# Optimization experiments

Measured on AMD Instinct MI355X. Metric: run time of the kernel, lower is better.

## Reference

```python
import jax, jax.numpy as jnp
import numpy as np
import math

D = 768
SCALE = math.sqrt(D)


def setup_inputs() -> dict:
    key = jax.random.key(0)
    k1, k2, k3, k4 = jax.random.split(key, 4)
    lhs = jax.random.normal(k1, (8, 1024, D), dtype=jnp.float32)
    rhs = jax.random.normal(k2, (8, 1024, D), dtype=jnp.float32)
    # xavier_normal_ std = sqrt(2/(fan_in+fan_out))
    std = math.sqrt(2.0 / (D + D))
    W_lhs = jax.random.normal(k3, (D, D), dtype=jnp.float32) * std
    W_rhs = jax.random.normal(k4, (D, D), dtype=jnp.float32) * std
    return {"lhs": lhs, "rhs": rhs, "W_lhs": W_lhs, "W_rhs": W_rhs}


def reference(lhs, rhs, W_lhs, W_rhs):
    # Linear (no bias): x @ W.T, then tanh
    l = jnp.tanh(jnp.einsum('nld,ed->nle', lhs, W_lhs))  # (N, L, D)
    r = jnp.tanh(jnp.einsum('nrd,ed->nre', rhs, W_rhs))  # (N, R, D)
    scores = jnp.einsum('nld,nrd->nlr', l, r)            # (N, L, R)
    attn_lhs = jax.nn.softmax(scores, axis=2)            # unscaled, row softmax
    attn_rhs = jax.nn.softmax(scores / SCALE, axis=1)    # scaled, column softmax
    out_lhs = jnp.einsum('nlr,nrd->nld', attn_lhs, rhs)
    out_rhs = jnp.einsum('nlr,nld->nrd', attn_rhs, lhs)
    return (jnp.concatenate([lhs, out_lhs], axis=2),
            jnp.concatenate([rhs, out_rhs], axis=2))
```

## Files before the change

kernel.cpp:

```cpp
#include <hip/hip_runtime.h>

typedef _Float16 f16_t;
typedef _Float16 f16x4 __attribute__((ext_vector_type(4)));
typedef _Float16 f16x8 __attribute__((ext_vector_type(8)));
typedef short s16x8 __attribute__((ext_vector_type(8)));
typedef unsigned short u16x4 __attribute__((ext_vector_type(4)));
typedef float floatx4 __attribute__((ext_vector_type(4)));

#define NB 8
#define SEQ 1024
#define DIM 768
#define INV_SCALE 0.03608439182435161f
#define ROW_SHIFT 40.0f

__device__ inline unsigned short f2bf(float f) {
  unsigned u = __builtin_bit_cast(unsigned, f);
  u += 0x7fffu + ((u >> 16) & 1u);
  return (unsigned short)(u >> 16);
}

__device__ inline void async_load16(const void* g, void* l) {
  __builtin_amdgcn_global_load_lds((__attribute__((address_space(1))) void*)g,
                                   (__attribute__((address_space(3))) void*)l,
                                   16, 0, 0);
}


__global__ __launch_bounds__(256) void prep(
    const float* __restrict__ lhs, const float* __restrict__ rhs,
    const float* __restrict__ Wl, const float* __restrict__ Wr,
    f16_t* __restrict__ lf, f16_t* __restrict__ rf, f16_t* __restrict__ lhsT,
    unsigned short* __restrict__ rhsT, f16_t* __restrict__ Wlh,
    f16_t* __restrict__ Wrh, float* __restrict__ o0, float* __restrict__ o1) {
  const int z = blockIdx.z;
  const int tid = threadIdx.x;
  const int x4 = (tid & 15) * 4, ty = tid >> 4;
  const int c0 = blockIdx.x * 64, r0 = blockIdx.y * 64;
  if (z >= 16) {
    if (blockIdx.y >= 12) return;
    const float* in = (z == 17 ? Wr : Wl);
    f16_t* out = (z == 17 ? Wrh : Wlh);
    #pragma unroll
    for (int it = 0; it < 4; ++it) {
      const int row = r0 + ty + it * 16;
      const float4 v = *(const float4*)&in[(size_t)row * DIM + c0 + x4];
      f16x4 h = {(f16_t)v.x, (f16_t)v.y, (f16_t)v.z, (f16_t)v.w};
      *(f16x4*)&out[(size_t)row * DIM + c0 + x4] = h;
    }
    return;
  }
  __shared__ float tile[64][65];
  const int n = z & 7;
  const float* in = (z < 8 ? lhs : rhs) + (size_t)n * SEQ * DIM;
  f16_t* fout = (z < 8 ? lf : rf) + (size_t)n * SEQ * DIM;
  float* oh = (z < 8 ? o0 : o1) + (size_t)n * SEQ * 2 * DIM;
  #pragma unroll
  for (int it = 0; it < 4; ++it) {
    const int row = ty + it * 16;
    const float4 v = *(const float4*)&in[(size_t)(r0 + row) * DIM + c0 + x4];
    f16x4 h = {(f16_t)v.x, (f16_t)v.y, (f16_t)v.z, (f16_t)v.w};
    *(f16x4*)&fout[(size_t)(r0 + row) * DIM + c0 + x4] = h;
    *(float4*)&oh[(size_t)(r0 + row) * 2 * DIM + c0 + x4] = v;
    tile[row][x4 + 0] = v.x;
    tile[row][x4 + 1] = v.y;
    tile[row][x4 + 2] = v.z;
    tile[row][x4 + 3] = v.w;
  }
  __syncthreads();
  if (z < 8) {
    f16_t* T = lhsT + (size_t)n * SEQ * DIM;
    #pragma unroll
    for (int it = 0; it < 4; ++it) {
      const int cr = ty + it * 16;
      f16x4 o = {(f16_t)tile[x4 + 0][cr], (f16_t)tile[x4 + 1][cr],
                 (f16_t)tile[x4 + 2][cr], (f16_t)tile[x4 + 3][cr]};
      *(f16x4*)&T[(size_t)(c0 + cr) * SEQ + r0 + x4] = o;
    }
  } else {
    unsigned short* T = rhsT + (size_t)n * SEQ * DIM;
    #pragma unroll
    for (int it = 0; it < 4; ++it) {
      const int cr = ty + it * 16;
      u16x4 o = {f2bf(tile[x4 + 0][cr]), f2bf(tile[x4 + 1][cr]),
                 f2bf(tile[x4 + 2][cr]), f2bf(tile[x4 + 3][cr])};
      *(u16x4*)&T[(size_t)(c0 + cr) * SEQ + r0 + x4] = o;
    }
  }
}

__global__ __launch_bounds__(256, 3) void gemm_proj(
    const f16_t* __restrict__ A0, const f16_t* __restrict__ W0,
    const f16_t* __restrict__ A1, const f16_t* __restrict__ W1,
    f16_t* __restrict__ C0, f16_t* __restrict__ C1) {
  __shared__ __align__(16) f16_t sA[128 * 64];
  __shared__ __align__(16) f16_t sB[128 * 64];
  const int b = blockIdx.x;
  const int n = b & 7;
  const int s = b >> 3;
  const int side = s / 48;
  const int t = s - side * 48;
  const int j = t >> 3, myb = t & 7;
  const int my = n * 8 + myb;
  const f16_t* Ab = (side ? A1 : A0) + (size_t)my * 128 * DIM;
  const f16_t* Bb = (side ? W1 : W0) + (size_t)j * 128 * DIM;
  f16_t* C = side ? C1 : C0;
  const int tid = threadIdx.x;
  const int lane = tid & 63;
  const int wave = tid >> 6;
  const int wr = wave >> 1, wc = wave & 1;
  const int fr = lane & 15;
  const int fq = lane >> 4;
  const int swz = ((lane & 7) ^ (lane >> 3)) << 3;
  const int x7 = (fr & 7) << 3;

  floatx4 acc[4][4] = {};

  for (int kt = 0; kt < DIM; kt += 64) {
    #pragma unroll
    for (int i = 0; i < 4; ++i) {
      const int ch = i * 4 + wave;
      const int row = ch * 8 + (lane >> 3);
      const size_t g = (size_t)row * DIM + kt + swz;
      async_load16(Ab + g, (char*)sA + ch * 1024);
      async_load16(Bb + g, (char*)sB + ch * 1024);
    }
    __syncthreads();
    #pragma unroll
    for (int ks = 0; ks < 64; ks += 32) {
      f16x8 af[4], bf[4];
      #pragma unroll
      for (int t2 = 0; t2 < 4; ++t2) {
        const int cs = (ks + fq * 8) ^ x7;
        af[t2] = *(const f16x8*)&sA[(wr * 64 + t2 * 16 + fr) * 64 + cs];
        bf[t2] = *(const f16x8*)&sB[(wc * 64 + t2 * 16 + fr) * 64 + cs];
      }
      #pragma unroll
      for (int ti = 0; ti < 4; ++ti)
        #pragma unroll
        for (int tj = 0; tj < 4; ++tj)
          acc[ti][tj] = __builtin_amdgcn_mfma_f32_16x16x32_f16(
              af[ti], bf[tj], acc[ti][tj], 0, 0, 0);
    }
    __syncthreads();
  }

  const size_t m0 = (size_t)my * 128, n0 = (size_t)j * 128;
  #pragma unroll
  for (int ti = 0; ti < 4; ++ti)
    #pragma unroll
    for (int tj = 0; tj < 4; ++tj) {
      const size_t gm = m0 + wr * 64 + ti * 16 + fq * 4;
      const size_t gn = n0 + wc * 64 + tj * 16 + fr;
      #pragma unroll
      for (int i = 0; i < 4; ++i) {
        const float e = __expf(2.f * acc[ti][tj][i]);
        C[(gm + i) * DIM + gn] =
            (f16_t)(1.f - 2.f * __builtin_amdgcn_rcpf(e + 1.f));
      }
    }
}

__global__ __launch_bounds__(256, 3) void gemm_scores(
    const f16_t* __restrict__ A, const f16_t* __restrict__ B,
    unsigned short* __restrict__ e_l, f16_t* __restrict__ e_rT,
    float* __restrict__ rowpart, float* __restrict__ colpart) {
  __shared__ __align__(16) char smem[32768];
  const int b = blockIdx.x;
  const int tid = threadIdx.x;
  f16_t* sA = (f16_t*)smem;
  f16_t* sB = sA + 8192;
  const int z = b & 7;
  const int s = b >> 3;
  const int my = s >> 3, j = s & 7;
  const f16_t* Ab = A + (size_t)z * SEQ * DIM + (size_t)my * 128 * DIM;
  const f16_t* Bb = B + (size_t)z * SEQ * DIM + (size_t)j * 128 * DIM;
  const int lane = tid & 63;
  const int wave = tid >> 6;
  const int wr = wave >> 1, wc = wave & 1;
  const int fr = lane & 15;
  const int fq = lane >> 4;
  const int swz = ((lane & 7) ^ (lane >> 3)) << 3;
  const int x7 = (fr & 7) << 3;

  floatx4 acc[4][4] = {};

  for (int kt = 0; kt < DIM; kt += 64) {
    #pragma unroll
    for (int i = 0; i < 4; ++i) {
      const int ch = i * 4 + wave;
      const int row = ch * 8 + (lane >> 3);
      const size_t g = (size_t)row * DIM + kt + swz;
      async_load16(Ab + g, (char*)sA + ch * 1024);
      async_load16(Bb + g, (char*)sB + ch * 1024);
    }
    __syncthreads();
    #pragma unroll
    for (int ks = 0; ks < 64; ks += 32) {
      f16x8 af[4], bf[4];
      #pragma unroll
      for (int t2 = 0; t2 < 4; ++t2) {
        const int cs = (ks + fq * 8) ^ x7;
        af[t2] = *(const f16x8*)&sA[(wr * 64 + t2 * 16 + fr) * 64 + cs];
        bf[t2] = *(const f16x8*)&sB[(wc * 64 + t2 * 16 + fr) * 64 + cs];
      }
      #pragma unroll
      for (int ti = 0; ti < 4; ++ti)
        #pragma unroll
        for (int tj = 0; tj < 4; ++tj)
          acc[ti][tj] = __builtin_amdgcn_mfma_f32_16x16x32_f16(
              af[ti], bf[tj], acc[ti][tj], 0, 0, 0);
    }
    __syncthreads();
  }

  const size_t m0 = (size_t)my * 128, n0 = (size_t)j * 128;
  unsigned short* eL = e_l + (size_t)z * SEQ * SEQ;
  f16_t* eT = e_rT + (size_t)z * SEQ * SEQ;

  #pragma unroll
  for (int ti = 0; ti < 4; ++ti) {
    #pragma unroll
    for (int i = 0; i < 4; ++i) {
      const int rloc = wr * 64 + ti * 16 + fq * 4 + i;
      float sum = 0.f;
      #pragma unroll
      for (int tj = 0; tj < 4; ++tj) {
        const float e = __expf(acc[ti][tj][i] - ROW_SHIFT);
        sum += e;
        eL[(m0 + rloc) * SEQ + n0 + wc * 64 + tj * 16 + fr] = f2bf(e);
      }
      sum += __shfl_xor(sum, 1, 64);
      sum += __shfl_xor(sum, 2, 64);
      sum += __shfl_xor(sum, 4, 64);
      sum += __shfl_xor(sum, 8, 64);
      if (fr == 0)
        rowpart[((size_t)(z * 16 + j * 2 + wc)) * SEQ + m0 + rloc] = sum;
    }
  }
  #pragma unroll
  for (int tj = 0; tj < 4; ++tj) {
    const int rp = wc * 64 + tj * 16 + fr;
    float sum = 0.f;
    #pragma unroll
    for (int ti = 0; ti < 4; ++ti) {
      #pragma unroll
      for (int i = 0; i < 4; ++i) {
        const float e = __expf(acc[ti][tj][i] * INV_SCALE);
        sum += e;
        const int cp = wr * 64 + ti * 16 + fq * 4 + i;
        *(f16_t*)(smem + rp * 256 + ((cp * 2) ^ ((rp & 7) << 4))) = (f16_t)e;
      }
    }
    sum += __shfl_xor(sum, 16, 64);
    sum += __shfl_xor(sum, 32, 64);
    if (fq == 0)
      colpart[((size_t)(z * 16 + my * 2 + wr)) * SEQ + n0 + rp] = sum;
  }
  __syncthreads();
  #pragma unroll
  for (int it = 0; it < 8; ++it) {
    const int r = it * 16 + (tid >> 4), chunk = tid & 15;
    const f16x8 v =
        *(const f16x8*)(smem + r * 256 + ((chunk * 16) ^ ((r & 7) << 4)));
    *(f16x8*)&eT[(n0 + r) * SEQ + m0 + chunk * 8] = v;
  }
}

template <bool BF>
__device__ __forceinline__ void apply_body(
    const f16_t* __restrict__ Ab, const f16_t* __restrict__ Bb,
    float* __restrict__ C, const float* __restrict__ pp, f16_t* sA, f16_t* sB,
    float* sinv) {
  const int tid = threadIdx.x;
  const int lane = tid & 63;
  const int wave = tid >> 6;
  const int wr = wave >> 1, wc = wave & 1;
  const int fr = lane & 15;
  const int fq = lane >> 4;
  const int swz = ((lane & 7) ^ (lane >> 3)) << 3;
  const int x7 = (fr & 7) << 3;

  if (tid < 128) {
    float s = 0.f;
    #pragma unroll
    for (int k = 0; k < 16; ++k) s += pp[k * SEQ + tid];
    sinv[tid] = 1.f / s;
  }

  floatx4 acc[4][4] = {};

  for (int kt = 0; kt < SEQ; kt += 64) {
    #pragma unroll
    for (int i = 0; i < 4; ++i) {
      const int ch = i * 4 + wave;
      const int row = ch * 8 + (lane >> 3);
      const size_t g = (size_t)row * SEQ + kt + swz;
      async_load16(Ab + g, (char*)sA + ch * 1024);
      async_load16(Bb + g, (char*)sB + ch * 1024);
    }
    __syncthreads();
    #pragma unroll
    for (int ks = 0; ks < 64; ks += 32) {
      const int cs = (ks + fq * 8) ^ x7;
      #pragma unroll
      for (int ti = 0; ti < 4; ++ti) {
        const f16_t* pa = &sA[(wr * 64 + ti * 16 + fr) * 64 + cs];
        #pragma unroll
        for (int tj = 0; tj < 4; ++tj) {
          const f16_t* pb = &sB[(wc * 64 + tj * 16 + fr) * 64 + cs];
          if constexpr (BF)
            acc[ti][tj] = __builtin_amdgcn_mfma_f32_16x16x32_bf16(
                *(const s16x8*)pa, *(const s16x8*)pb, acc[ti][tj], 0, 0, 0);
          else
            acc[ti][tj] = __builtin_amdgcn_mfma_f32_16x16x32_f16(
                *(const f16x8*)pa, *(const f16x8*)pb, acc[ti][tj], 0, 0, 0);
        }
      }
    }
    __syncthreads();
  }

  #pragma unroll
  for (int ti = 0; ti < 4; ++ti) {
    const int gm = wr * 64 + ti * 16 + fq * 4;
    const floatx4 iv = *(const floatx4*)&sinv[gm];
    #pragma unroll
    for (int tj = 0; tj < 4; ++tj) {
      const int gn = wc * 64 + tj * 16 + fr;
      #pragma unroll
      for (int i = 0; i < 4; ++i)
        C[(size_t)(gm + i) * (2 * DIM) + gn] = acc[ti][tj][i] * iv[i];
    }
  }
}

__global__ __launch_bounds__(256, 3) void gemm_apply(
    const f16_t* __restrict__ e_l, const f16_t* __restrict__ e_rT,
    const f16_t* __restrict__ rhsT, const f16_t* __restrict__ lhsT,
    const float* __restrict__ rowpart, const float* __restrict__ colpart,
    float* __restrict__ out0, float* __restrict__ out1) {
  __shared__ __align__(16) f16_t sA[128 * 64];
  __shared__ __align__(16) f16_t sB[128 * 64];
  __shared__ __align__(16) float sinv[128];
  const int b = blockIdx.x;
  const int n = b & 7;
  const int s = b >> 3;
  const int side = s / 48;
  const int t = s - side * 48;
  const int j = t >> 3, my = t & 7;
  const size_t m0 = (size_t)my * 128, n0 = (size_t)j * 128;
  if (side == 0) {
    apply_body<true>(e_l + (size_t)n * SEQ * SEQ + m0 * SEQ,
                     rhsT + (size_t)n * SEQ * DIM + n0 * SEQ,
                     out0 + (size_t)n * SEQ * 2 * DIM + DIM + m0 * 2 * DIM + n0,
                     rowpart + (size_t)n * 16 * SEQ + m0, sA, sB, sinv);
  } else {
    apply_body<false>(
        e_rT + (size_t)n * SEQ * SEQ + m0 * SEQ,
        lhsT + (size_t)n * SEQ * DIM + n0 * SEQ,
        out1 + (size_t)n * SEQ * 2 * DIM + DIM + m0 * 2 * DIM + n0,
        colpart + (size_t)n * 16 * SEQ + m0, sA, sB, sinv);
  }
}

extern "C" void kernel_launch(void* const* d_in, const int* in_sizes, int n_in,
                              void* d_out, int out_size, void* d_ws,
                              size_t ws_size, hipStream_t stream) {
  const float* lhs = (const float*)d_in[0];
  const float* rhs = (const float*)d_in[1];
  const float* Wl = (const float*)d_in[2];
  const float* Wr = (const float*)d_in[3];
  float* out0 = (float*)d_out;
  float* out1 = out0 + (size_t)NB * SEQ * (2 * DIM);

  char* ws = (char*)d_ws;
  f16_t* lhsT = (f16_t*)(ws + 0);
  unsigned short* rhsT = (unsigned short*)(ws + 12582912);
  f16_t* l_f = (f16_t*)(ws + 25165824);
  f16_t* r_f = (f16_t*)(ws + 37748736);
  f16_t* lhs_f = (f16_t*)(ws + 50331648);
  f16_t* rhs_f = (f16_t*)(ws + 62914560);
  f16_t* Wl_h = (f16_t*)(ws + 75497472);
  f16_t* Wr_h = (f16_t*)(ws + 76677120);
  unsigned short* e_l = (unsigned short*)(ws + 50331648);
  f16_t* e_rT = (f16_t*)(ws + 67108864);
  float* rowpart = (float*)(ws + 83886080);
  float* colpart = (float*)(ws + 84410368);

  prep<<<dim3(12, 16, 18), 256, 0, stream>>>(lhs, rhs, Wl, Wr, lhs_f, rhs_f,
                                             lhsT, rhsT, Wl_h, Wr_h, out0,
                                             out1);
  gemm_proj<<<768, 256, 0, stream>>>(lhs_f, Wl_h, rhs_f, Wr_h, l_f, r_f);
  gemm_scores<<<512, 256, 0, stream>>>(l_f, r_f, e_l, e_rT, rowpart, colpart);
  gemm_apply<<<768, 256, 0, stream>>>((const f16_t*)e_l, e_rT,
                                      (const f16_t*)rhsT, lhsT, rowpart,
                                      colpart, out0, out1);
}
```

Before: 233.9 us.

## Fuse four kernels into one persistent megakernel with grid barriers

Result: slower. 515.5 us (+120.4%).

```diff
diff --git a/kernel.cpp b/kernel.cpp
--- a/kernel.cpp
+++ b/kernel.cpp
@@ -10,6 +10,7 @@
 #define NB 8
 #define SEQ 1024
 #define DIM 768
+#define NBLK 768
 #define INV_SCALE 0.03608439182435161f
 #define ROW_SHIFT 40.0f
 
@@ -25,85 +26,35 @@
                                    16, 0, 0);
 }
 
-
-__global__ __launch_bounds__(256) void prep(
+__device__ inline void grid_barrier(unsigned* sync, int phase) {
+  __syncthreads();
+  if (threadIdx.x == 0) {
+    __threadfence();
+    const unsigned arrived = atomicAdd(&sync[phase * 2], 1u);
+    if (arrived == NBLK - 1) {
+      atomicExch(&sync[phase * 2 + 1], 1u);
+    } else {
+      while (atomicOr(&sync[phase * 2 + 1], 0u) == 0u)
+        __builtin_amdgcn_s_sleep(8);
+    }
+    __threadfence();
+  }
+  __syncthreads();
+}
+
+__global__ __launch_bounds__(256, 3) void mega(
     const float* __restrict__ lhs, const float* __restrict__ rhs,
     const float* __restrict__ Wl, const float* __restrict__ Wr,
-    f16_t* __restrict__ lf, f16_t* __restrict__ rf, f16_t* __restrict__ lhsT,
-    unsigned short* __restrict__ rhsT, f16_t* __restrict__ Wlh,
-    f16_t* __restrict__ Wrh, float* __restrict__ o0, float* __restrict__ o1) {
-  const int z = blockIdx.z;
-  const int tid = threadIdx.x;
-  const int x4 = (tid & 15) * 4, ty = tid >> 4;
-  const int c0 = blockIdx.x * 64, r0 = blockIdx.y * 64;
-  if (z >= 16) {
-    if (blockIdx.y >= 12) return;
-    const float* in = (z == 17 ? Wr : Wl);
-    f16_t* out = (z == 17 ? Wrh : Wlh);
-    #pragma unroll
-    for (int it = 0; it < 4; ++it) {
-      const int row = r0 + ty + it * 16;
-      const float4 v = *(const float4*)&in[(size_t)row * DIM + c0 + x4];
-      f16x4 h = {(f16_t)v.x, (f16_t)v.y, (f16_t)v.z, (f16_t)v.w};
-      *(f16x4*)&out[(size_t)row * DIM + c0 + x4] = h;
-    }
-    return;
-  }
-  __shared__ float tile[64][65];
-  const int n = z & 7;
-  const float* in = (z < 8 ? lhs : rhs) + (size_t)n * SEQ * DIM;
-  f16_t* fout = (z < 8 ? lf : rf) + (size_t)n * SEQ * DIM;
-  float* oh = (z < 8 ? o0 : o1) + (size_t)n * SEQ * 2 * DIM;
-  #pragma unroll
-  for (int it = 0; it < 4; ++it) {
-    const int row = ty + it * 16;
-    const float4 v = *(const float4*)&in[(size_t)(r0 + row) * DIM + c0 + x4];
-    f16x4 h = {(f16_t)v.x, (f16_t)v.y, (f16_t)v.z, (f16_t)v.w};
-    *(f16x4*)&fout[(size_t)(r0 + row) * DIM + c0 + x4] = h;
-    *(float4*)&oh[(size_t)(r0 + row) * 2 * DIM + c0 + x4] = v;
-    tile[row][x4 + 0] = v.x;
-    tile[row][x4 + 1] = v.y;
-    tile[row][x4 + 2] = v.z;
-    tile[row][x4 + 3] = v.w;
-  }
-  __syncthreads();
-  if (z < 8) {
-    f16_t* T = lhsT + (size_t)n * SEQ * DIM;
-    #pragma unroll
-    for (int it = 0; it < 4; ++it) {
-      const int cr = ty + it * 16;
-      f16x4 o = {(f16_t)tile[x4 + 0][cr], (f16_t)tile[x4 + 1][cr],
-                 (f16_t)tile[x4 + 2][cr], (f16_t)tile[x4 + 3][cr]};
-      *(f16x4*)&T[(size_t)(c0 + cr) * SEQ + r0 + x4] = o;
-    }
-  } else {
-    unsigned short* T = rhsT + (size_t)n * SEQ * DIM;
-    #pragma unroll
-    for (int it = 0; it < 4; ++it) {
-      const int cr = ty + it * 16;
-      u16x4 o = {f2bf(tile[x4 + 0][cr]), f2bf(tile[x4 + 1][cr]),
-                 f2bf(tile[x4 + 2][cr]), f2bf(tile[x4 + 3][cr])};
-      *(u16x4*)&T[(size_t)(c0 + cr) * SEQ + r0 + x4] = o;
-    }
-  }
-}
-
-__global__ __launch_bounds__(256, 3) void gemm_proj(
-    const f16_t* __restrict__ A0, const f16_t* __restrict__ W0,
-    const f16_t* __restrict__ A1, const f16_t* __restrict__ W1,
-    f16_t* __restrict__ C0, f16_t* __restrict__ C1) {
-  __shared__ __align__(16) f16_t sA[128 * 64];
-  __shared__ __align__(16) f16_t sB[128 * 64];
-  const int b = blockIdx.x;
-  const int n = b & 7;
-  const int s = b >> 3;
-  const int side = s / 48;
-  const int t = s - side * 48;
-  const int j = t >> 3, myb = t & 7;
-  const int my = n * 8 + myb;
-  const f16_t* Ab = (side ? A1 : A0) + (size_t)my * 128 * DIM;
-  const f16_t* Bb = (side ? W1 : W0) + (size_t)j * 128 * DIM;
-  f16_t* C = side ? C1 : C0;
+    f16_t* __restrict__ lhs_f, f16_t* __restrict__ rhs_f,
+    f16_t* __restrict__ Wl_h, f16_t* __restrict__ Wr_h,
+    f16_t* __restrict__ lhsT, unsigned short* __restrict__ rhsT,
+    f16_t* __restrict__ l_f, f16_t* __restrict__ r_f,
+    unsigned short* __restrict__ e_l, f16_t* __restrict__ e_rT,
+    float* __restrict__ rowpart, float* __restrict__ colpart,
+    float* __restrict__ out0, float* __restrict__ out1, unsigned* sync) {
+  __shared__ __align__(16) char smem[32768];
+  __shared__ __align__(16) float sinv[128];
+  const int bid = blockIdx.x;
   const int tid = threadIdx.x;
   const int lane = tid & 63;
   const int wave = tid >> 6;
@@ -113,253 +64,290 @@
   const int swz = ((lane & 7) ^ (lane >> 3)) << 3;
   const int x7 = (fr & 7) << 3;
 
-  floatx4 acc[4][4] = {};
-
-  for (int kt = 0; kt < DIM; kt += 64) {
-    #pragma unroll
-    for (int i = 0; i < 4; ++i) {
-      const int ch = i * 4 + wave;
-      const int row = ch * 8 + (lane >> 3);
-      const size_t g = (size_t)row * DIM + kt + swz;
-      async_load16(Ab + g, (char*)sA + ch * 1024);
-      async_load16(Bb + g, (char*)sB + ch * 1024);
+  {
+    const int x4 = (tid & 15) * 4, ty = tid >> 4;
+    float(*tile)[65] = (float(*)[65])smem;
+    for (int v = bid; v < 3456; v += NBLK) {
+      const int z = v / 192;
+      const int rem = v - z * 192;
+      const int by = rem / 12, bx = rem - by * 12;
+      const int c0 = bx * 64, r0 = by * 64;
+      if (z >= 16) {
+        if (by < 12) {
+          const float* in = (z == 17 ? Wr : Wl);
+          f16_t* outp = (z == 17 ? Wr_h : Wl_h);
+          #pragma unroll
+          for (int it = 0; it < 4; ++it) {
+            const int row = r0 + ty + it * 16;
+            const float4 v4 = *(const float4*)&in[(size_t)row * DIM + c0 + x4];
+            *(f16x4*)&outp[(size_t)row * DIM + c0 + x4] =
+                f16x4{(f16_t)v4.x, (f16_t)v4.y, (f16_t)v4.z, (f16_t)v4.w};
+          }
+        }
+      } else {
+        const int n = z & 7;
+        const float* in = (z < 8 ? lhs : rhs) + (size_t)n * SEQ * DIM;
+        f16_t* fout = (z < 8 ? lhs_f : rhs_f) + (size_t)n * SEQ * DIM;
+        float* oh = (z < 8 ? out0 : out1) + (size_t)n * SEQ * 2 * DIM;
+        #pragma unroll
+        for (int it = 0; it < 4; ++it) {
+          const int row = ty + it * 16;
+          const float4 v4 =
+              *(const float4*)&in[(size_t)(r0 + row) * DIM + c0 + x4];
+          *(f16x4*)&fout[(size_t)(r0 + row) * DIM + c0 + x4] =
+              f16x4{(f16_t)v4.x, (f16_t)v4.y, (f16_t)v4.z, (f16_t)v4.w};
+          *(float4*)&oh[(size_t)(r0 + row) * 2 * DIM + c0 + x4] = v4;
+          tile[row][x4 + 0] = v4.x;
+          tile[row][x4 + 1] = v4.y;
+          tile[row][x4 + 2] = v4.z;
+          tile[row][x4 + 3] = v4.w;
+        }
+        __syncthreads();
+        if (z < 8) {
+          f16_t* T = lhsT + (size_t)n * SEQ * DIM;
+          #pragma unroll
+          for (int it = 0; it < 4; ++it) {
+            const int cr = ty + it * 16;
+            f16x4 o = {(f16_t)tile[x4 + 0][cr], (f16_t)tile[x4 + 1][cr],
+                       (f16_t)tile[x4 + 2][cr], (f16_t)tile[x4 + 3][cr]};
+            *(f16x4*)&T[(size_t)(c0 + cr) * SEQ + r0 + x4] = o;
+          }
+        } else {
+          unsigned short* T = rhsT + (size_t)n * SEQ * DIM;
+          #pragma unroll
+          for (int it = 0; it < 4; ++it) {
+            const int cr = ty + it * 16;
+            u16x4 o = {f2bf(tile[x4 + 0][cr]), f2bf(tile[x4 + 1][cr]),
+                       f2bf(tile[x4 + 2][cr]), f2bf(tile[x4 + 3][cr])};
+            *(u16x4*)&T[(size_t)(c0 + cr) * SEQ + r0 + x4] = o;
+          }
+        }
+      }
+      __syncthreads();
+    }
+  }
+  grid_barrier(sync, 0);
+
+  {
+    f16_t* sA = (f16_t*)smem;
+    f16_t* sB = sA + 8192;
+    const int n = bid & 7;
+    const int s = bid >> 3;
+    const int side = s / 48;
+    const int t = s - side * 48;
+    const int j = t >> 3, myb = t & 7;
+    const int my = n * 8 + myb;
+    const f16_t* Ab = (side ? rhs_f : lhs_f) + (size_t)my * 128 * DIM;
+    const f16_t* Bb = (side ? Wr_h : Wl_h) + (size_t)j * 128 * DIM;
+    f16_t* C = side ? r_f : l_f;
+
+    floatx4 acc[4][4] = {};
+    for (int kt = 0; kt < DIM; kt += 64) {
+      #pragma unroll
+      for (int i = 0; i < 4; ++i) {
+        const int ch = i * 4 + wave;
+        const int row = ch * 8 + (lane >> 3);
+        const size_t g = (size_t)row * DIM + kt + swz;
+        async_load16(Ab + g, (char*)sA + ch * 1024);
+        async_load16(Bb + g, (char*)sB + ch * 1024);
+      }
+      __syncthreads();
+      #pragma unroll
+      for (int ks = 0; ks < 64; ks += 32) {
+        f16x8 af[4], bf[4];
+        #pragma unroll
+        for (int t2 = 0; t2 < 4; ++t2) {
+          const int cs = (ks + fq * 8) ^ x7;
+          af[t2] = *(const f16x8*)&sA[(wr * 64 + t2 * 16 + fr) * 64 + cs];
+          bf[t2] = *(const f16x8*)&sB[(wc * 64 + t2 * 16 + fr) * 64 + cs];
+        }
+        #pragma unroll
+        for (int ti = 0; ti < 4; ++ti)
+          #pragma unroll
+          for (int tj = 0; tj < 4; ++tj)
+            acc[ti][tj] = __builtin_amdgcn_mfma_f32_16x16x32_f16(
+                af[ti], bf[tj], acc[ti][tj], 0, 0, 0);
+      }
+      __syncthreads();
+    }
+    const size_t m0 = (size_t)my * 128, n0 = (size_t)j * 128;
+    #pragma unroll
+    for (int ti = 0; ti < 4; ++ti)
+      #pragma unroll
+      for (int tj = 0; tj < 4; ++tj) {
+        const size_t gm = m0 + wr * 64 + ti * 16 + fq * 4;
+        const size_t gn = n0 + wc * 64 + tj * 16 + fr;
+        #pragma unroll
+        for (int i = 0; i < 4; ++i) {
+          const float e = __expf(2.f * acc[ti][tj][i]);
+          C[(gm + i) * DIM + gn] =
+              (f16_t)(1.f - 2.f * __builtin_amdgcn_rcpf(e + 1.f));
+        }
+      }
+  }
+  grid_barrier(sync, 1);
+
+  if (bid < 512) {
+    f16_t* sA = (f16_t*)smem;
+    f16_t* sB = sA + 8192;
+    const int z = bid & 7;
+    const int s = bid >> 3;
+    const int my = s >> 3, j = s & 7;
+    const f16_t* Ab = l_f + (size_t)z * SEQ * DIM + (size_t)my * 128 * DIM;
+    const f16_t* Bb = r_f + (size_t)z * SEQ * DIM + (size_t)j * 128 * DIM;
+
+    floatx4 acc[4][4] = {};
+    for (int kt = 0; kt < DIM; kt += 64) {
+      #pragma unroll
+      for (int i = 0; i < 4; ++i) {
+        const int ch = i * 4 + wave;
+        const int row = ch * 8 + (lane >> 3);
+        const size_t g = (size_t)row * DIM + kt + swz;
+        async_load16(Ab + g, (char*)sA + ch * 1024);
+        async_load16(Bb + g, (char*)sB + ch * 1024);
+      }
+      __syncthreads();
+      #pragma unroll
+      for (int ks = 0; ks < 64; ks += 32) {
+        f16x8 af[4], bf[4];
+        #pragma unroll
+        for (int t2 = 0; t2 < 4; ++t2) {
+          const int cs = (ks + fq * 8) ^ x7;
+          af[t2] = *(const f16x8*)&sA[(wr * 64 + t2 * 16 + fr) * 64 + cs];
+          bf[t2] = *(const f16x8*)&sB[(wc * 64 + t2 * 16 + fr) * 64 + cs];
+        }
+        #pragma unroll
+        for (int ti = 0; ti < 4; ++ti)
+          #pragma unroll
+          for (int tj = 0; tj < 4; ++tj)
+            acc[ti][tj] = __builtin_amdgcn_mfma_f32_16x16x32_f16(
+                af[ti], bf[tj], acc[ti][tj], 0, 0, 0);
+      }
+      __syncthreads();
+    }
+
+    const size_t m0 = (size_t)my * 128, n0 = (size_t)j * 128;
+    unsigned short* eL = e_l + (size_t)z * SEQ * SEQ;
+    f16_t* eT = e_rT + (size_t)z * SEQ * SEQ;
+
+    #pragma unroll
+    for (int ti = 0; ti < 4; ++ti) {
+      #pragma unroll
+      for (int i = 0; i < 4; ++i) {
+        const int rloc = wr * 64 + ti * 16 + fq * 4 + i;
+        float sum = 0.f;
+        #pragma unroll
+        for (int tj = 0; tj < 4; ++tj) {
+          const float e = __expf(acc[ti][tj][i] - ROW_SHIFT);
+          sum += e;
+          eL[(m0 + rloc) * SEQ + n0 + wc * 64 + tj * 16 + fr] = f2bf(e);
+        }
+        sum += __shfl_xor(sum, 1, 64);
+        sum += __shfl_xor(sum, 2, 64);
+        sum += __shfl_xor(sum, 4, 64);
+        sum += __shfl_xor(sum, 8, 64);
+        if (fr == 0)
+          rowpart[((size_t)(z * 16 + j * 2 + wc)) * SEQ + m0 + rloc] = sum;
+      }
+    }
+    #pragma unroll
+    for (int tj = 0; tj < 4; ++tj) {
+      const int rp = wc * 64 + tj * 16 + fr;
+      float sum = 0.f;
+      #pragma unroll
+      for (int ti = 0; ti < 4; ++ti) {
+        #pragma unroll
+        for (int i = 0; i < 4; ++i) {
+          const float e = __expf(acc[ti][tj][i] * INV_SCALE);
+          sum += e;
+          const int cp = wr * 64 + ti * 16 + fq * 4 + i;
+          *(f16_t*)(smem + rp * 256 + ((cp * 2) ^ ((rp & 7) << 4))) = (f16_t)e;
+        }
+      }
+      sum += __shfl_xor(sum, 16, 64);
+      sum += __shfl_xor(sum, 32, 64);
+      if (fq == 0)
+        colpart[((size_t)(z * 16 + my * 2 + wr)) * SEQ + n0 + rp] = sum;
     }
     __syncthreads();
     #pragma unroll
-    for (int ks = 0; ks < 64; ks += 32) {
-      f16x8 af[4], bf[4];
-      #pragma unroll
-      for (int t2 = 0; t2 < 4; ++t2) {
+    for (int it = 0; it < 8; ++it) {
+      const int r = it * 16 + (tid >> 4), chunk = tid & 15;
+      const f16x8 v =
+          *(const f16x8*)(smem + r * 256 + ((chunk * 16) ^ ((r & 7) << 4)));
+      *(f16x8*)&eT[(n0 + r) * SEQ + m0 + chunk * 8] = v;
+    }
+  }
+  grid_barrier(sync, 2);
+
+  {
+    f16_t* sA = (f16_t*)smem;
+    f16_t* sB = sA + 8192;
+    const int n = bid & 7;
+    const int s = bid >> 3;
+    const int side = s / 48;
+    const int t = s - side * 48;
+    const int j = t >> 3, my = t & 7;
+    const size_t m0 = (size_t)my * 128, n0 = (size_t)j * 128;
+    const f16_t* Ab = (side ? e_rT : (const f16_t*)e_l) +
+                      (size_t)n * SEQ * SEQ + m0 * SEQ;
+    const f16_t* Bb = (side ? lhsT : (const f16_t*)rhsT) +
+                      (size_t)n * SEQ * DIM + n0 * SEQ;
+    float* C = (side ? out1 : out0) + (size_t)n * SEQ * 2 * DIM + DIM +
+               m0 * 2 * DIM + n0;
+    const float* pp = (side ? colpart : rowpart) + (size_t)n * 16 * SEQ + m0;
+
+    if (tid < 128) {
+      float ssum = 0.f;
+      #pragma unroll
+      for (int k = 0; k < 16; ++k) ssum += pp[k * SEQ + tid];
+      sinv[tid] = 1.f / ssum;
+    }
+
+    floatx4 acc[4][4] = {};
+    for (int kt = 0; kt < SEQ; kt += 64) {
+      #pragma unroll
+      for (int i = 0; i < 4; ++i) {
+        const int ch = i * 4 + wave;
+        const int row = ch * 8 + (lane >> 3);
+        const size_t g = (size_t)row * SEQ + kt + swz;
+        async_load16(Ab + g, (char*)sA + ch * 1024);
+        async_load16(Bb + g, (char*)sB + ch * 1024);
+      }
+      __syncthreads();
+      #pragma unroll
+      for (int ks = 0; ks < 64; ks += 32) {
         const int cs = (ks + fq * 8) ^ x7;
-        af[t2] = *(const f16x8*)&sA[(wr * 64 + t2 * 16 + fr) * 64 + cs];
-        bf[t2] = *(const f16x8*)&sB[(wc * 64 + t2 * 16 + fr) * 64 + cs];
-      }
-      #pragma unroll
-      for (int ti = 0; ti < 4; ++ti)
-        #pragma unroll
-        for (int tj = 0; tj < 4; ++tj)
-          acc[ti][tj] = __builtin_amdgcn_mfma_f32_16x16x32_f16(
-              af[ti], bf[tj], acc[ti][tj], 0, 0, 0);
-    }
-    __syncthreads();
-  }
-
-  const size_t m0 = (size_t)my * 128, n0 = (size_t)j * 128;
-  #pragma unroll
-  for (int ti = 0; ti < 4; ++ti)
-    #pragma unroll
-    for (int tj = 0; tj < 4; ++tj) {
-      const size_t gm = m0 + wr * 64 + ti * 16 + fq * 4;
-      const size_t gn = n0 + wc * 64 + tj * 16 + fr;
-      #pragma unroll
-      for (int i = 0; i < 4; ++i) {
-        const float e = __expf(2.f * acc[ti][tj][i]);
-        C[(gm + i) * DIM + gn] =
-            (f16_t)(1.f - 2.f * __builtin_amdgcn_rcpf(e + 1.f));
-      }
-    }
-}
-
-__global__ __launch_bounds__(256, 3) void gemm_scores(
-    const f16_t* __restrict__ A, const f16_t* __restrict__ B,
-    unsigned short* __restrict__ e_l, f16_t* __restrict__ e_rT,
-    float* __restrict__ rowpart, float* __restrict__ colpart) {
-  __shared__ __align__(16) char smem[32768];
-  const int b = blockIdx.x;
-  const int tid = threadIdx.x;
-  f16_t* sA = (f16_t*)smem;
-  f16_t* sB = sA + 8192;
-  const int z = b & 7;
-  const int s = b >> 3;
-  const int my = s >> 3, j = s & 7;
-  const f16_t* Ab = A + (size_t)z * SEQ * DIM + (size_t)my * 128 * DIM;
-  const f16_t* Bb = B + (size_t)z * SEQ * DIM + (size_t)j * 128 * DIM;
-  const int lane = tid & 63;
-  const int wave = tid >> 6;
-  const int wr = wave >> 1, wc = wave & 1;
-  const int fr = lane & 15;
-  const int fq = lane >> 4;
-  const int swz = ((lane & 7) ^ (lane >> 3)) << 3;
-  const int x7 = (fr & 7) << 3;
-
-  floatx4 acc[4][4] = {};
-
-  for (int kt = 0; kt < DIM; kt += 64) {
-    #pragma unroll
-    for (int i = 0; i < 4; ++i) {
-      const int ch = i * 4 + wave;
-      const int row = ch * 8 + (lane >> 3);
-      const size_t g = (size_t)row * DIM + kt + swz;
-      async_load16(Ab + g, (char*)sA + ch * 1024);
-      async_load16(Bb + g, (char*)sB + ch * 1024);
-    }
-    __syncthreads();
-    #pragma unroll
-    for (int ks = 0; ks < 64; ks += 32) {
-      f16x8 af[4], bf[4];
-      #pragma unroll
-      for (int t2 = 0; t2 < 4; ++t2) {
-        const int cs = (ks + fq * 8) ^ x7;
-        af[t2] = *(const f16x8*)&sA[(wr * 64 + t2 * 16 + fr) * 64 + cs];
-        bf[t2] = *(const f16x8*)&sB[(wc * 64 + t2 * 16 + fr) * 64 + cs];
-      }
-      #pragma unroll
-      for (int ti = 0; ti < 4; ++ti)
-        #pragma unroll
-        for (int tj = 0; tj < 4; ++tj)
-          acc[ti][tj] = __builtin_amdgcn_mfma_f32_16x16x32_f16(
-              af[ti], bf[tj], acc[ti][tj], 0, 0, 0);
-    }
-    __syncthreads();
-  }
-
-  const size_t m0 = (size_t)my * 128, n0 = (size_t)j * 128;
-  unsigned short* eL = e_l + (size_t)z * SEQ * SEQ;
-  f16_t* eT = e_rT + (size_t)z * SEQ * SEQ;
-
-  #pragma unroll
-  for (int ti = 0; ti < 4; ++ti) {
-    #pragma unroll
-    for (int i = 0; i < 4; ++i) {
-      const int rloc = wr * 64 + ti * 16 + fq * 4 + i;
-      float sum = 0.f;
+        #pragma unroll
+        for (int ti = 0; ti < 4; ++ti) {
+          const f16_t* pa = &sA[(wr * 64 + ti * 16 + fr) * 64 + cs];
+          #pragma unroll
+          for (int tj = 0; tj < 4; ++tj) {
+            const f16_t* pb = &sB[(wc * 64 + tj * 16 + fr) * 64 + cs];
+            if (side == 0)
+              acc[ti][tj] = __builtin_amdgcn_mfma_f32_16x16x32_bf16(
+                  *(const s16x8*)pa, *(const s16x8*)pb, acc[ti][tj], 0, 0, 0);
+            else
+              acc[ti][tj] = __builtin_amdgcn_mfma_f32_16x16x32_f16(
+                  *(const f16x8*)pa, *(const f16x8*)pb, acc[ti][tj], 0, 0, 0);
+          }
+        }
+      }
+      __syncthreads();
+    }
+
+    #pragma unroll
+    for (int ti = 0; ti < 4; ++ti) {
+      const int gm = wr * 64 + ti * 16 + fq * 4;
+      const floatx4 iv = *(const floatx4*)&sinv[gm];
       #pragma unroll
       for (int tj = 0; tj < 4; ++tj) {
-        const float e = __expf(acc[ti][tj][i] - ROW_SHIFT);
-        sum += e;
-        eL[(m0 + rloc) * SEQ + n0 + wc * 64 + tj * 16 + fr] = f2bf(e);
-      }
-      sum += __shfl_xor(sum, 1, 64);
-      sum += __shfl_xor(sum, 2, 64);
-      sum += __shfl_xor(sum, 4, 64);
-      sum += __shfl_xor(sum, 8, 64);
-      if (fr == 0)
-        rowpart[((size_t)(z * 16 + j * 2 + wc)) * SEQ + m0 + rloc] = sum;
-    }
-  }
-  #pragma unroll
-  for (int tj = 0; tj < 4; ++tj) {
-    const int rp = wc * 64 + tj * 16 + fr;
-    float sum = 0.f;
-    #pragma unroll
-    for (int ti = 0; ti < 4; ++ti) {
-      #pragma unroll
-      for (int i = 0; i < 4; ++i) {
-        const float e = __expf(acc[ti][tj][i] * INV_SCALE);
-        sum += e;
-        const int cp = wr * 64 + ti * 16 + fq * 4 + i;
-        *(f16_t*)(smem + rp * 256 + ((cp * 2) ^ ((rp & 7) << 4))) = (f16_t)e;
-      }
-    }
-    sum += __shfl_xor(sum, 16, 64);
-    sum += __shfl_xor(sum, 32, 64);
-    if (fq == 0)
-      colpart[((size_t)(z * 16 + my * 2 + wr)) * SEQ + n0 + rp] = sum;
-  }
-  __syncthreads();
-  #pragma unroll
-  for (int it = 0; it < 8; ++it) {
-    const int r = it * 16 + (tid >> 4), chunk = tid & 15;
-    const f16x8 v =
-        *(const f16x8*)(smem + r * 256 + ((chunk * 16) ^ ((r & 7) << 4)));
-    *(f16x8*)&eT[(n0 + r) * SEQ + m0 + chunk * 8] = v;
-  }
-}
-
-template <bool BF>
-__device__ __forceinline__ void apply_body(
-    const f16_t* __restrict__ Ab, const f16_t* __restrict__ Bb,
-    float* __restrict__ C, const float* __restrict__ pp, f16_t* sA, f16_t* sB,
-    float* sinv) {
-  const int tid = threadIdx.x;
-  const int lane = tid & 63;
-  const int wave = tid >> 6;
-  const int wr = wave >> 1, wc = wave & 1;
-  const int fr = lane & 15;
-  const int fq = lane >> 4;
-  const int swz = ((lane & 7) ^ (lane >> 3)) << 3;
-  const int x7 = (fr & 7) << 3;
-
-  if (tid < 128) {
-    float s = 0.f;
-    #pragma unroll
-    for (int k = 0; k < 16; ++k) s += pp[k * SEQ + tid];
-    sinv[tid] = 1.f / s;
-  }
-
-  floatx4 acc[4][4] = {};
-
-  for (int kt = 0; kt < SEQ; kt += 64) {
-    #pragma unroll
-    for (int i = 0; i < 4; ++i) {
-      const int ch = i * 4 + wave;
-      const int row = ch * 8 + (lane >> 3);
-      const size_t g = (size_t)row * SEQ + kt + swz;
-      async_load16(Ab + g, (char*)sA + ch * 1024);
-      async_load16(Bb + g, (char*)sB + ch * 1024);
-    }
-    __syncthreads();
-    #pragma unroll
-    for (int ks = 0; ks < 64; ks += 32) {
-      const int cs = (ks + fq * 8) ^ x7;
-      #pragma unroll
-      for (int ti = 0; ti < 4; ++ti) {
-        const f16_t* pa = &sA[(wr * 64 + ti * 16 + fr) * 64 + cs];
-        #pragma unroll
-        for (int tj = 0; tj < 4; ++tj) {
-          const f16_t* pb = &sB[(wc * 64 + tj * 16 + fr) * 64 + cs];
-          if constexpr (BF)
-            acc[ti][tj] = __builtin_amdgcn_mfma_f32_16x16x32_bf16(
-                *(const s16x8*)pa, *(const s16x8*)pb, acc[ti][tj], 0, 0, 0);
-          else
-            acc[ti][tj] = __builtin_amdgcn_mfma_f32_16x16x32_f16(
-                *(const f16x8*)pa, *(const f16x8*)pb, acc[ti][tj], 0, 0, 0);
-        }
-      }
-    }
-    __syncthreads();
-  }
-
-  #pragma unroll
-  for (int ti = 0; ti < 4; ++ti) {
-    const int gm = wr * 64 + ti * 16 + fq * 4;
-    const floatx4 iv = *(const floatx4*)&sinv[gm];
-    #pragma unroll
-    for (int tj = 0; tj < 4; ++tj) {
-      const int gn = wc * 64 + tj * 16 + fr;
-      #pragma unroll
-      for (int i = 0; i < 4; ++i)
-        C[(size_t)(gm + i) * (2 * DIM) + gn] = acc[ti][tj][i] * iv[i];
-    }
-  }
-}
-
-__global__ __launch_bounds__(256, 3) void gemm_apply(
-    const f16_t* __restrict__ e_l, const f16_t* __restrict__ e_rT,
-    const f16_t* __restrict__ rhsT, const f16_t* __restrict__ lhsT,
-    const float* __restrict__ rowpart, const float* __restrict__ colpart,
-    float* __restrict__ out0, float* __restrict__ out1) {
-  __shared__ __align__(16) f16_t sA[128 * 64];
-  __shared__ __align__(16) f16_t sB[128 * 64];
-  __shared__ __align__(16) float sinv[128];
-  const int b = blockIdx.x;
-  const int n = b & 7;
-  const int s = b >> 3;
-  const int side = s / 48;
-  const int t = s - side * 48;
-  const int j = t >> 3, my = t & 7;
-  const size_t m0 = (size_t)my * 128, n0 = (size_t)j * 128;
-  if (side == 0) {
-    apply_body<true>(e_l + (size_t)n * SEQ * SEQ + m0 * SEQ,
-                     rhsT + (size_t)n * SEQ * DIM + n0 * SEQ,
-                     out0 + (size_t)n * SEQ * 2 * DIM + DIM + m0 * 2 * DIM + n0,
-                     rowpart + (size_t)n * 16 * SEQ + m0, sA, sB, sinv);
-  } else {
-    apply_body<false>(
-        e_rT + (size_t)n * SEQ * SEQ + m0 * SEQ,
-        lhsT + (size_t)n * SEQ * DIM + n0 * SEQ,
-        out1 + (size_t)n * SEQ * 2 * DIM + DIM + m0 * 2 * DIM + n0,
-        colpart + (size_t)n * 16 * SEQ + m0, sA, sB, sinv);
+        const int gn = wc * 64 + tj * 16 + fr;
+        #pragma unroll
+        for (int i = 0; i < 4; ++i)
+          C[(size_t)(gm + i) * (2 * DIM) + gn] = acc[ti][tj][i] * iv[i];
+      }
+    }
   }
 }
 
@@ -386,13 +374,10 @@
   f16_t* e_rT = (f16_t*)(ws + 67108864);
   float* rowpart = (float*)(ws + 83886080);
   float* colpart = (float*)(ws + 84410368);
-
-  prep<<<dim3(12, 16, 18), 256, 0, stream>>>(lhs, rhs, Wl, Wr, lhs_f, rhs_f,
-                                             lhsT, rhsT, Wl_h, Wr_h, out0,
-                                             out1);
-  gemm_proj<<<768, 256, 0, stream>>>(lhs_f, Wl_h, rhs_f, Wr_h, l_f, r_f);
-  gemm_scores<<<512, 256, 0, stream>>>(l_f, r_f, e_l, e_rT, rowpart, colpart);
-  gemm_apply<<<768, 256, 0, stream>>>((const f16_t*)e_l, e_rT,
-                                      (const f16_t*)rhsT, lhsT, rowpart,
-                                      colpart, out0, out1);
-}
+  unsigned* sync = (unsigned*)(ws + 84934656);
+
+  hipMemsetAsync(sync, 0, 64, stream);
+  mega<<<NBLK, 256, 0, stream>>>(lhs, rhs, Wl, Wr, lhs_f, rhs_f, Wl_h, Wr_h,
+                                 lhsT, rhsT, l_f, r_f, e_l, e_rT, rowpart,
+                                 colpart, out0, out1, sync);
+}
```
